# Kernel tuning notes

Measured on AMD Instinct MI355X. Metric: run time of the kernel, lower is better.

The kernel has to match this reference:

```python
import jax, jax.numpy as jnp
import numpy as np

D_MODEL = 1024
NUM_HEADS = 16
HEAD_DIM = D_MODEL // NUM_HEADS
BATCH = 4
SEQ = 2048


def circulant(x, c, b):
    # Circulant linear layer via FFT: y = irfft(rfft(x) * rfft(c)) + b
    # x: (..., d), c: (d,), b: (d,)
    d = c.shape[0]
    y = jnp.fft.irfft(jnp.fft.rfft(x, axis=-1) * jnp.fft.rfft(c), n=d, axis=-1)
    return y + b


def setup_inputs() -> dict:
    key = jax.random.key(0)
    ks = jax.random.split(key, 9)
    scale = 1.0 / np.sqrt(D_MODEL)
    inp = {
        "x": jax.random.normal(ks[0], (BATCH, SEQ, D_MODEL), dtype=jnp.float32),
        "wq_c": jax.random.normal(ks[1], (D_MODEL,), dtype=jnp.float32) * scale,
        "wq_b": jnp.zeros((D_MODEL,), dtype=jnp.float32),
        "wk_c": jax.random.normal(ks[2], (D_MODEL,), dtype=jnp.float32) * scale,
        "wk_b": jnp.zeros((D_MODEL,), dtype=jnp.float32),
        "wv_c": jax.random.normal(ks[3], (D_MODEL,), dtype=jnp.float32) * scale,
        "wv_b": jnp.zeros((D_MODEL,), dtype=jnp.float32),
        "wo_c": jax.random.normal(ks[4], (D_MODEL,), dtype=jnp.float32) * scale,
        "wo_b": jnp.zeros((D_MODEL,), dtype=jnp.float32),
    }
    return inp


def reference(x, wq_c, wq_b, wk_c, wk_b, wv_c, wv_b, wo_c, wo_b):
    bs, seq_len, dm = x.shape
    Q = circulant(x, wq_c, wq_b)  # (B, S, D)
    K = circulant(x, wk_c, wk_b)
    V = circulant(x, wv_c, wv_b)
    Q = Q.reshape(bs, seq_len, NUM_HEADS, HEAD_DIM)
    K = K.reshape(bs, seq_len, NUM_HEADS, HEAD_DIM)
    V = V.reshape(bs, seq_len, NUM_HEADS, HEAD_DIM)
    scale = HEAD_DIM ** (-0.5)
    attn_logits = jnp.einsum("bqhd,bkhd->bhqk", Q, K) * scale  # (B, H, S, S)
    attn_weights = jax.nn.softmax(attn_logits, axis=-1)
    out_heads = jnp.einsum("bhqk,bkhd->bqhd", attn_weights, V)
    out_merge = out_heads.reshape(bs, seq_len, dm)
    out = circulant(out_merge, wo_c, wo_b)
    return out
```

## Files before the change

### kernel.cpp

```cpp
#include <hip/hip_runtime.h>
#include <hip/hip_bf16.h>

#define D_MODEL 1024
#define NUM_HEADS 16
#define HEAD_DIM 64
#define BATCH 4
#define SEQ 2048
#define MROWS (BATCH * SEQ)

using f32x4  = __attribute__((ext_vector_type(4))) float;
using bf16x8 = __attribute__((ext_vector_type(8))) short;
using short4v = __attribute__((ext_vector_type(4))) short;

__device__ inline unsigned short f2bf(float f) {
    __hip_bfloat16 h = __float2bfloat16(f);
    return *reinterpret_cast<unsigned short*>(&h);
}

__device__ inline void gld_lds16(const unsigned short* g, unsigned short* l) {
    __builtin_amdgcn_global_load_lds(
        (const __attribute__((address_space(1))) unsigned int*)g,
        (__attribute__((address_space(3))) unsigned int*)l, 16, 0, 0);
}

#define QSCALE 0.18033688011112042f

__global__ __launch_bounds__(256) void build_w(
    const float* __restrict__ cq, const float* __restrict__ ck,
    const float* __restrict__ cv, const float* __restrict__ co,
    const float* __restrict__ bq, const float* __restrict__ bk,
    const float* __restrict__ bv, const float* __restrict__ bo,
    unsigned short* __restrict__ Wt, float* __restrict__ bias)
{
    const int n = blockIdx.x;
    const int sel = n >> 10, nl = n & 1023;
    const float* c  = sel == 0 ? cq : sel == 1 ? ck : sel == 2 ? cv : co;
    const float* bb = sel == 0 ? bq : sel == 1 ? bk : sel == 2 ? bv : bo;
    const float sc = (sel == 0) ? QSCALE : 1.0f;
    const int t = threadIdx.x;
    ushort4 o;
    o.x = f2bf(sc * c[(nl - (4*t + 0)) & 1023]);
    o.y = f2bf(sc * c[(nl - (4*t + 1)) & 1023]);
    o.z = f2bf(sc * c[(nl - (4*t + 2)) & 1023]);
    o.w = f2bf(sc * c[(nl - (4*t + 3)) & 1023]);
    ((ushort4*)(Wt + (size_t)n * 1024))[t] = o;
    if (t == 0) bias[n] = sc * bb[nl];
}

__global__ __launch_bounds__(256) void xcast(
    const float* __restrict__ x, unsigned short* __restrict__ xb)
{
    const size_t i = (size_t)blockIdx.x * 1024 + threadIdx.x * 4;
    float4 v = *(const float4*)(x + i);
    ushort4 o;
    o.x = f2bf(v.x); o.y = f2bf(v.y); o.z = f2bf(v.z); o.w = f2bf(v.w);
    *(ushort4*)(xb + i) = o;
}

template <int OUT_MODE>
__global__ __launch_bounds__(256, 3) void gemm_circ(
    const unsigned short* __restrict__ A,
    const unsigned short* __restrict__ Bt,
    const float* __restrict__ bias,
    unsigned short* __restrict__ Qb, unsigned short* __restrict__ Kb,
    unsigned short* __restrict__ Vt, float* __restrict__ Cf)
{
    __shared__ unsigned short As[128 * 64];
    __shared__ unsigned short Bs[128 * 64];
    const int t = threadIdx.x;
    const int w = t >> 6, lane = t & 63;
    const int quad = lane >> 4, l16 = lane & 15;
    const int m0 = blockIdx.x * 128;
    const int n0 = blockIdx.y * 128;
    const int wm = (w & 1) * 64, wn = (w >> 1) * 64;

    f32x4 acc[4][4];
#pragma unroll
    for (int i = 0; i < 4; ++i)
#pragma unroll
        for (int j = 0; j < 4; ++j) acc[i][j] = (f32x4){0.f, 0.f, 0.f, 0.f};

    for (int k0 = 0; k0 < 1024; k0 += 64) {
        __syncthreads();
#pragma unroll
        for (int j = 0; j < 4; ++j) {
            const int s = j * 4 + w;
            const int i = s * 64 + lane;
            const int r = i >> 3;
            const int c = (i & 7) ^ (r & 7);
            gld_lds16(A  + (size_t)(m0 + r) * 1024 + k0 + c * 8, &As[s * 512]);
            gld_lds16(Bt + (size_t)(n0 + r) * 1024 + k0 + c * 8, &Bs[s * 512]);
        }
        __syncthreads();

#pragma unroll
        for (int kk = 0; kk < 2; ++kk) {
            bf16x8 af[4], bfr[4];
#pragma unroll
            for (int i = 0; i < 4; ++i) {
                const int r = wm + i * 16 + l16;
                const int slot = r * 8 + ((kk * 4 + quad) ^ (r & 7));
                af[i] = *(const bf16x8*)&As[slot * 8];
            }
#pragma unroll
            for (int j = 0; j < 4; ++j) {
                const int r = wn + j * 16 + l16;
                const int slot = r * 8 + ((kk * 4 + quad) ^ (r & 7));
                bfr[j] = *(const bf16x8*)&Bs[slot * 8];
            }
#pragma unroll
            for (int i = 0; i < 4; ++i)
#pragma unroll
                for (int j = 0; j < 4; ++j)
                    acc[i][j] = __builtin_amdgcn_mfma_f32_16x16x32_bf16(
                        af[i], bfr[j], acc[i][j], 0, 0, 0);
        }
    }

#pragma unroll
    for (int i = 0; i < 4; ++i) {
        const int gm = m0 + wm + i * 16 + quad * 4;
#pragma unroll
        for (int j = 0; j < 4; ++j) {
            const int gn = n0 + wn + j * 16 + l16;
            const float bv = bias[gn];
            if (OUT_MODE == 1) {
#pragma unroll
                for (int rr = 0; rr < 4; ++rr)
                    Cf[(size_t)(gm + rr) * 1024 + gn] = acc[i][j][rr] + bv;
            } else {
                const int sel = gn >> 10;
                if (sel == 0) {
#pragma unroll
                    for (int rr = 0; rr < 4; ++rr)
                        Qb[(size_t)(gm + rr) * 1024 + gn] = f2bf(acc[i][j][rr] + bv);
                } else if (sel == 1) {
                    const int col = gn & 1023;
#pragma unroll
                    for (int rr = 0; rr < 4; ++rr)
                        Kb[(size_t)(gm + rr) * 1024 + col] = f2bf(acc[i][j][rr] + bv);
                } else {
                    const int d = gn & 1023;
                    const int head = d >> 6, dl = d & 63;
                    const int b = gm >> 11, key = gm & 2047;
                    ushort4 vv;
                    vv.x = f2bf(acc[i][j][0] + bv);
                    vv.y = f2bf(acc[i][j][1] + bv);
                    vv.z = f2bf(acc[i][j][2] + bv);
                    vv.w = f2bf(acc[i][j][3] + bv);
                    *(ushort4*)&Vt[((size_t)((b * 16 + head) * 64 + dl)) * 2048 + key] = vv;
                }
            }
        }
    }
}

union PUn { uint2 u2; short4v s4; };

__global__ __launch_bounds__(256, 2) void attn_mfma(
    const unsigned short* __restrict__ Qb, const unsigned short* __restrict__ Kb,
    const unsigned short* __restrict__ Vt, unsigned short* __restrict__ O)
{
    __shared__ unsigned short Ks[2][64 * 64];
    __shared__ unsigned short Vs[2][64 * 64];
    __shared__ unsigned short Ps[4][64 * 64];

    const int t = threadIdx.x;
    const int w = t >> 6, lane = t & 63;
    const int quad = lane >> 4, l16 = lane & 15;
    const int qh = quad >> 1, ql = quad & 1;
    const int bh = blockIdx.x;
    const int b = bh >> 4, head = bh & 15;
    const int qbase = blockIdx.y * 256 + w * 64;

    bf16x8 qa[4][2];
#pragma unroll
    for (int s = 0; s < 4; ++s)
#pragma unroll
        for (int h = 0; h < 2; ++h) {
            size_t off = (size_t)(b * SEQ + qbase + s*16 + l16) * D_MODEL
                       + head * HEAD_DIM + h*32 + quad*8;
            qa[s][h] = *(const bf16x8*)(Qb + off);
        }

    f32x4 acc[4][4];
#pragma unroll
    for (int s = 0; s < 4; ++s)
#pragma unroll
        for (int dt = 0; dt < 4; ++dt) acc[s][dt] = (f32x4){0.f,0.f,0.f,0.f};
    float lp[4] = {0.f, 0.f, 0.f, 0.f};

    const size_t kbase  = (size_t)(b * SEQ) * D_MODEL + head * HEAD_DIM;
    const size_t vtbase = (size_t)((b * NUM_HEADS + head) * HEAD_DIM) * SEQ;
    unsigned short* Pw = Ps[w];

#pragma unroll
    for (int j = 0; j < 2; ++j) {
        const int seg = j * 4 + w;
        const int i = seg * 64 + lane;
        const int r = i >> 3;
        const int c = (i & 7) ^ (r & 7);
        gld_lds16(Kb + kbase + (size_t)r * D_MODEL + c * 8, &Ks[0][seg * 512]);
        gld_lds16(Vt + vtbase + (size_t)r * SEQ + c * 8, &Vs[0][seg * 512]);
    }

    int ib = 0;
    for (int kb = 0; kb < SEQ; kb += 64, ib ^= 1) {
        __syncthreads();

        if (kb + 64 < SEQ) {
#pragma unroll
            for (int j = 0; j < 2; ++j) {
                const int seg = j * 4 + w;
                const int i = seg * 64 + lane;
                const int r = i >> 3;
                const int c = (i & 7) ^ (r & 7);
                gld_lds16(Kb + kbase + (size_t)(kb + 64 + r) * D_MODEL + c * 8,
                          &Ks[ib ^ 1][seg * 512]);
                gld_lds16(Vt + vtbase + (size_t)r * SEQ + kb + 64 + c * 8,
                          &Vs[ib ^ 1][seg * 512]);
            }
        }

        bf16x8 kf[4][2];
#pragma unroll
        for (int kt = 0; kt < 4; ++kt) {
            const int r = kt * 16 + l16;
#pragma unroll
            for (int h = 0; h < 2; ++h) {
                const int c = (h * 4 + quad) ^ (r & 7);
                kf[kt][h] = *(const bf16x8*)&Ks[ib][(r * 8 + c) * 8];
            }
        }

#pragma unroll
        for (int s = 0; s < 4; ++s) {
            f32x4 st[4];
#pragma unroll
            for (int kt = 0; kt < 4; ++kt) st[kt] = (f32x4){0.f,0.f,0.f,0.f};
#pragma unroll
            for (int kt = 0; kt < 4; ++kt)
#pragma unroll
                for (int h = 0; h < 2; ++h)
                    st[kt] = __builtin_amdgcn_mfma_f32_16x16x32_bf16(
                        kf[kt][h], qa[s][h], st[kt], 0, 0, 0);

            const int q = s * 16 + l16;
            unsigned short* qrow = &Pw[q * 64];
#pragma unroll
            for (int kt = 0; kt < 4; ++kt) {
                float p0 = __builtin_amdgcn_exp2f(st[kt][0]);
                float p1 = __builtin_amdgcn_exp2f(st[kt][1]);
                float p2 = __builtin_amdgcn_exp2f(st[kt][2]);
                float p3 = __builtin_amdgcn_exp2f(st[kt][3]);
                lp[s] += (p0 + p1) + (p2 + p3);
                __hip_bfloat162 lo = __float22bfloat162_rn(make_float2(p0, p1));
                __hip_bfloat162 hi = __float22bfloat162_rn(make_float2(p2, p3));
                PUn pu;
                pu.u2.x = *reinterpret_cast<unsigned int*>(&lo);
                pu.u2.y = *reinterpret_cast<unsigned int*>(&hi);
                const int chunk = (kt * 2 + qh) ^ (q & 7);
                *(short4v*)&qrow[chunk * 8 + ql * 4] = pu.s4;
            }
        }

        __asm__ __volatile__("" ::: "memory");
        __builtin_amdgcn_s_waitcnt(0xC07F);
        __asm__ __volatile__("" ::: "memory");

#pragma unroll
        for (int kh = 0; kh < 2; ++kh) {
            bf16x8 pf[4];
#pragma unroll
            for (int s = 0; s < 4; ++s) {
                const int q = s * 16 + l16;
                const int c = (kh * 4 + quad) ^ (q & 7);
                pf[s] = *(const bf16x8*)&Pw[(q * 8 + c) * 8];
            }
#pragma unroll
            for (int dt = 0; dt < 4; ++dt) {
                const int r = dt * 16 + l16;
                const int cv = (kh * 4 + quad) ^ (r & 7);
                bf16x8 vf = *(const bf16x8*)&Vs[ib][(r * 8 + cv) * 8];
#pragma unroll
                for (int s = 0; s < 4; ++s)
                    acc[s][dt] = __builtin_amdgcn_mfma_f32_16x16x32_bf16(
                        pf[s], vf, acc[s][dt], 0, 0, 0);
            }
        }
    }

#pragma unroll
    for (int s = 0; s < 4; ++s) {
        lp[s] += __shfl_xor(lp[s], 16);
        lp[s] += __shfl_xor(lp[s], 32);
    }

#pragma unroll
    for (int s = 0; s < 4; ++s)
#pragma unroll
        for (int rr = 0; rr < 4; ++rr) {
            float denom = __shfl(lp[s], quad * 4 + rr);
            float inv = 1.0f / denom;
            int q = qbase + s*16 + quad*4 + rr;
            unsigned short* orow = O + (size_t)(b * SEQ + q) * D_MODEL + head * HEAD_DIM + l16;
#pragma unroll
            for (int dt = 0; dt < 4; ++dt) orow[dt*16] = f2bf(acc[s][dt][rr] * inv);
        }
}

extern "C" void kernel_launch(void* const* d_in, const int* in_sizes, int n_in,
                              void* d_out, int out_size, void* d_ws, size_t ws_size,
                              hipStream_t stream) {
    const float* x    = (const float*)d_in[0];
    const float* wq_c = (const float*)d_in[1];
    const float* wq_b = (const float*)d_in[2];
    const float* wk_c = (const float*)d_in[3];
    const float* wk_b = (const float*)d_in[4];
    const float* wv_c = (const float*)d_in[5];
    const float* wv_b = (const float*)d_in[6];
    const float* wo_c = (const float*)d_in[7];
    const float* wo_b = (const float*)d_in[8];
    float* out = (float*)d_out;

    char* ws = (char*)d_ws;
    unsigned short* Wt   = (unsigned short*)(ws);
    float*          bias = (float*)(ws + ((size_t)8  << 20));
    unsigned short* xb   = (unsigned short*)(ws + ((size_t)10 << 20));
    unsigned short* Qb   = (unsigned short*)(ws + ((size_t)26 << 20));
    unsigned short* Kb   = (unsigned short*)(ws + ((size_t)42 << 20));
    unsigned short* Vt   = (unsigned short*)(ws + ((size_t)58 << 20));
    unsigned short* Ob   = (unsigned short*)(ws + ((size_t)74 << 20));

    build_w<<<4096, 256, 0, stream>>>(wq_c, wk_c, wv_c, wo_c,
                                      wq_b, wk_b, wv_b, wo_b, Wt, bias);
    xcast<<<MROWS, 256, 0, stream>>>(x, xb);
    gemm_circ<0><<<dim3(64, 24), 256, 0, stream>>>(xb, Wt, bias, Qb, Kb, Vt, nullptr);
    attn_mfma<<<dim3(BATCH * NUM_HEADS, SEQ / 256), 256, 0, stream>>>(Qb, Kb, Vt, Ob);
    gemm_circ<1><<<dim3(64, 8), 256, 0, stream>>>(Ob, Wt + (size_t)3072 * 1024,
                                                  bias + 3072, nullptr, nullptr, nullptr, out);
}
```

Baseline: 252.0 us.

## Keep softmax probabilities in registers by permuting K rows to match MFMA layout

Removes the per-warp LDS staging buffer for P, along with its stores, the waitcnt barrier and the reloads. K rows are loaded into MFMA fragments in a permuted order, with a matching swizzle, so the QK^T accumulator output lines up directly with the A-operand layout the PV MFMA needs. This cuts LDS traffic and frees 32KB of shared memory per block. In exchange the exp and convert work is interleaved differently and the K swizzle pattern is more complex, which may change bank-conflict behaviour.

```diff
diff --git a/kernel.cpp b/kernel.cpp
--- a/kernel.cpp
+++ b/kernel.cpp
@@ -155,20 +155,16 @@
     }
 }
 
-union PUn { uint2 u2; short4v s4; };
-
 __global__ __launch_bounds__(256, 2) void attn_mfma(
     const unsigned short* __restrict__ Qb, const unsigned short* __restrict__ Kb,
     const unsigned short* __restrict__ Vt, unsigned short* __restrict__ O)
 {
     __shared__ unsigned short Ks[2][64 * 64];
     __shared__ unsigned short Vs[2][64 * 64];
-    __shared__ unsigned short Ps[4][64 * 64];
 
     const int t = threadIdx.x;
     const int w = t >> 6, lane = t & 63;
     const int quad = lane >> 4, l16 = lane & 15;
-    const int qh = quad >> 1, ql = quad & 1;
     const int bh = blockIdx.x;
     const int b = bh >> 4, head = bh & 15;
     const int qbase = blockIdx.y * 256 + w * 64;
@@ -192,16 +188,16 @@
 
     const size_t kbase  = (size_t)(b * SEQ) * D_MODEL + head * HEAD_DIM;
     const size_t vtbase = (size_t)((b * NUM_HEADS + head) * HEAD_DIM) * SEQ;
-    unsigned short* Pw = Ps[w];
 
 #pragma unroll
     for (int j = 0; j < 2; ++j) {
         const int seg = j * 4 + w;
         const int i = seg * 64 + lane;
         const int r = i >> 3;
-        const int c = (i & 7) ^ (r & 7);
-        gld_lds16(Kb + kbase + (size_t)r * D_MODEL + c * 8, &Ks[0][seg * 512]);
-        gld_lds16(Vt + vtbase + (size_t)r * SEQ + c * 8, &Vs[0][seg * 512]);
+        const int ck = (i & 7) ^ ((r & 3) | ((r >> 1) & 4));
+        const int cv = (i & 7) ^ (r & 7);
+        gld_lds16(Kb + kbase + (size_t)r * D_MODEL + ck * 8, &Ks[0][seg * 512]);
+        gld_lds16(Vt + vtbase + (size_t)r * SEQ + cv * 8, &Vs[0][seg * 512]);
     }
 
     int ib = 0;
@@ -214,69 +210,64 @@
                 const int seg = j * 4 + w;
                 const int i = seg * 64 + lane;
                 const int r = i >> 3;
-                const int c = (i & 7) ^ (r & 7);
-                gld_lds16(Kb + kbase + (size_t)(kb + 64 + r) * D_MODEL + c * 8,
+                const int ck = (i & 7) ^ ((r & 3) | ((r >> 1) & 4));
+                const int cv = (i & 7) ^ (r & 7);
+                gld_lds16(Kb + kbase + (size_t)(kb + 64 + r) * D_MODEL + ck * 8,
                           &Ks[ib ^ 1][seg * 512]);
-                gld_lds16(Vt + vtbase + (size_t)r * SEQ + kb + 64 + c * 8,
+                gld_lds16(Vt + vtbase + (size_t)r * SEQ + kb + 64 + cv * 8,
                           &Vs[ib ^ 1][seg * 512]);
             }
         }
 
-        bf16x8 kf[4][2];
-#pragma unroll
-        for (int kt = 0; kt < 4; ++kt) {
-            const int r = kt * 16 + l16;
-#pragma unroll
-            for (int h = 0; h < 2; ++h) {
-                const int c = (h * 4 + quad) ^ (r & 7);
-                kf[kt][h] = *(const bf16x8*)&Ks[ib][(r * 8 + c) * 8];
-            }
-        }
-
-#pragma unroll
-        for (int s = 0; s < 4; ++s) {
-            f32x4 st[4];
-#pragma unroll
-            for (int kt = 0; kt < 4; ++kt) st[kt] = (f32x4){0.f,0.f,0.f,0.f};
-#pragma unroll
-            for (int kt = 0; kt < 4; ++kt)
-#pragma unroll
-                for (int h = 0; h < 2; ++h)
-                    st[kt] = __builtin_amdgcn_mfma_f32_16x16x32_bf16(
-                        kf[kt][h], qa[s][h], st[kt], 0, 0, 0);
-
-            const int q = s * 16 + l16;
-            unsigned short* qrow = &Pw[q * 64];
-#pragma unroll
-            for (int kt = 0; kt < 4; ++kt) {
-                float p0 = __builtin_amdgcn_exp2f(st[kt][0]);
-                float p1 = __builtin_amdgcn_exp2f(st[kt][1]);
-                float p2 = __builtin_amdgcn_exp2f(st[kt][2]);
-                float p3 = __builtin_amdgcn_exp2f(st[kt][3]);
-                lp[s] += (p0 + p1) + (p2 + p3);
-                __hip_bfloat162 lo = __float22bfloat162_rn(make_float2(p0, p1));
-                __hip_bfloat162 hi = __float22bfloat162_rn(make_float2(p2, p3));
-                PUn pu;
-                pu.u2.x = *reinterpret_cast<unsigned int*>(&lo);
-                pu.u2.y = *reinterpret_cast<unsigned int*>(&hi);
-                const int chunk = (kt * 2 + qh) ^ (q & 7);
-                *(short4v*)&qrow[chunk * 8 + ql * 4] = pu.s4;
-            }
-        }
-
-        __asm__ __volatile__("" ::: "memory");
-        __builtin_amdgcn_s_waitcnt(0xC07F);
-        __asm__ __volatile__("" ::: "memory");
+        bf16x8 kf[2][2][2];
+#pragma unroll
+        for (int kh = 0; kh < 2; ++kh)
+#pragma unroll
+            for (int m = 0; m < 2; ++m) {
+                const int r = kh * 32 + ((l16 >> 2) << 3) + m * 4 + (l16 & 3);
+                const int sg = (r & 3) | ((r >> 1) & 4);
+#pragma unroll
+                for (int h = 0; h < 2; ++h) {
+                    const int cc = (h * 4 + quad) ^ sg;
+                    kf[kh][m][h] = *(const bf16x8*)&Ks[ib][(r * 8 + cc) * 8];
+                }
+            }
 
 #pragma unroll
         for (int kh = 0; kh < 2; ++kh) {
             bf16x8 pf[4];
 #pragma unroll
             for (int s = 0; s < 4; ++s) {
-                const int q = s * 16 + l16;
-                const int c = (kh * 4 + quad) ^ (q & 7);
-                pf[s] = *(const bf16x8*)&Pw[(q * 8 + c) * 8];
-            }
+                f32x4 st0 = (f32x4){0.f,0.f,0.f,0.f};
+                f32x4 st1 = (f32x4){0.f,0.f,0.f,0.f};
+#pragma unroll
+                for (int h = 0; h < 2; ++h) {
+                    st0 = __builtin_amdgcn_mfma_f32_16x16x32_bf16(
+                        kf[kh][0][h], qa[s][h], st0, 0, 0, 0);
+                    st1 = __builtin_amdgcn_mfma_f32_16x16x32_bf16(
+                        kf[kh][1][h], qa[s][h], st1, 0, 0, 0);
+                }
+                float p0 = __builtin_amdgcn_exp2f(st0[0]);
+                float p1 = __builtin_amdgcn_exp2f(st0[1]);
+                float p2 = __builtin_amdgcn_exp2f(st0[2]);
+                float p3 = __builtin_amdgcn_exp2f(st0[3]);
+                float p4 = __builtin_amdgcn_exp2f(st1[0]);
+                float p5 = __builtin_amdgcn_exp2f(st1[1]);
+                float p6 = __builtin_amdgcn_exp2f(st1[2]);
+                float p7 = __builtin_amdgcn_exp2f(st1[3]);
+                lp[s] += ((p0 + p1) + (p2 + p3)) + ((p4 + p5) + (p6 + p7));
+                __hip_bfloat162 w0 = __float22bfloat162_rn(make_float2(p0, p1));
+                __hip_bfloat162 w1 = __float22bfloat162_rn(make_float2(p2, p3));
+                __hip_bfloat162 w2 = __float22bfloat162_rn(make_float2(p4, p5));
+                __hip_bfloat162 w3 = __float22bfloat162_rn(make_float2(p6, p7));
+                union { bf16x8 v; unsigned int u[4]; } pu;
+                pu.u[0] = *reinterpret_cast<unsigned int*>(&w0);
+                pu.u[1] = *reinterpret_cast<unsigned int*>(&w1);
+                pu.u[2] = *reinterpret_cast<unsigned int*>(&w2);
+                pu.u[3] = *reinterpret_cast<unsigned int*>(&w3);
+                pf[s] = pu.v;
+            }
+
 #pragma unroll
             for (int dt = 0; dt < 4; ++dt) {
                 const int r = dt * 16 + l16;
```

Result: faster. 247.0 us (-2.0%).
